# Kernel optimization log

Measured on AMD Instinct MI355X. Metric: run time of the kernel, lower is better.

Reference implementation:

```python
import jax, jax.numpy as jnp
import numpy as np

B, H, S, D = 4, 16, 2048, 64
DROPOUT_P = 0.5
INV_SCALE = np.sqrt(DROPOUT_P)  # module quirk: divides qk by sqrt(dropout_p)


def setup_inputs() -> dict:
    key = jax.random.key(0)
    kq, kk, kv, km = jax.random.split(key, 4)
    query = jax.random.normal(kq, (B, H, S, D), dtype=jnp.float32)
    key_t = jax.random.normal(kk, (B, H, S, D), dtype=jnp.float32)
    value = jax.random.normal(kv, (B, H, S, D), dtype=jnp.float32)
    # inverted dropout mask: keep with prob (1-p), scale kept entries by 1/(1-p)
    u = jax.random.uniform(km, (B, H, S, S), dtype=jnp.float32)
    dropout_mask = (u > DROPOUT_P).astype(jnp.float32) / (1.0 - DROPOUT_P)
    return {"query": query, "key_t": key_t, "value": value, "dropout_mask": dropout_mask}


def reference(query, key_t, value, dropout_mask):
    # qk = Q @ K^T, scaled by 1/inv_scale_factor  (inv_scale_factor = sqrt(0.5))
    qk = jnp.einsum("bhsd,bhtd->bhst", query, key_t) / INV_SCALE
    attn = jax.nn.softmax(qk, axis=-1)
    attn = attn * dropout_mask  # fused dropout (training mode, p=0.5)
    out = jnp.einsum("bhst,bhtd->bhsd", attn, value)
    return out
```

## Files before the change

### kernel.cpp

```cpp
#include <hip/hip_runtime.h>

#define Bn 4
#define Hn 16
#define Sn 2048
#define Dn 64
#define NT (Sn / 64)
#define BLOB 24576
#define WS_NEED ((size_t)Bn * Hn * NT * BLOB)

typedef __attribute__((ext_vector_type(8))) short bf16x8;
typedef __attribute__((ext_vector_type(4))) float f32x4;
typedef __attribute__((ext_vector_type(4))) float float4_t;

__device__ __forceinline__ short f2bf(float f) {
    union { float f; unsigned u; } v; v.f = f;
    unsigned r = v.u + 0x7fffu + ((v.u >> 16) & 1u);
    return (short)(r >> 16);
}
__device__ __forceinline__ float bf2f(short h) {
    union { unsigned u; float f; } v; v.u = ((unsigned)(unsigned short)h) << 16;
    return v.f;
}

__global__ __launch_bounds__(256) void prepass_kernel(
    const float* __restrict__ K, const float* __restrict__ V, char* __restrict__ ws)
{
    const int tid = threadIdx.x;
    const int kv0 = (blockIdx.x & (NT - 1)) * 64;
    char* blob = ws + (size_t)blockIdx.x * BLOB;
    const size_t kv_base = (size_t)(blockIdx.x >> 5) * Sn * Dn;

    {
        const int r  = tid >> 2;
        const int dc = (tid & 3) * 16;
        const float* krow = K + kv_base + (size_t)(kv0 + r) * Dn + dc;
        float4_t k0 = ((const float4_t*)krow)[0];
        float4_t k1 = ((const float4_t*)krow)[1];
        float4_t k2 = ((const float4_t*)krow)[2];
        float4_t k3 = ((const float4_t*)krow)[3];
        float fv[16] = {k0[0],k0[1],k0[2],k0[3], k1[0],k1[1],k1[2],k1[3],
                        k2[0],k2[1],k2[2],k2[3], k3[0],k3[1],k3[2],k3[3]};
        bf16x8 ha, hb, la, lb;
#pragma unroll
        for (int j = 0; j < 8; ++j) {
            short h = f2bf(fv[j]);
            ha[j] = h; la[j] = f2bf(fv[j] - bf2f(h));
            short h2 = f2bf(fv[j + 8]);
            hb[j] = h2; lb[j] = f2bf(fv[j + 8] - bf2f(h2));
        }
        const unsigned base = (unsigned)(r * 128 + dc * 2);
        const unsigned swz  = (unsigned)((r & 7) << 4);
        *(bf16x8*)(blob + ((base) ^ swz))             = ha;
        *(bf16x8*)(blob + ((base + 16) ^ swz))        = hb;
        *(bf16x8*)(blob + 8192 + ((base) ^ swz))      = la;
        *(bf16x8*)(blob + 8192 + ((base + 16) ^ swz)) = lb;
    }
    {
        const int r2 = (tid & 31) * 2;
        const int d0 = (tid >> 5) * 8;
        const float* v0 = V + kv_base + (size_t)(kv0 + r2) * Dn + d0;
        float4_t a0 = ((const float4_t*)v0)[0];
        float4_t a1 = ((const float4_t*)v0)[1];
        float4_t b0 = ((const float4_t*)(v0 + Dn))[0];
        float4_t b1 = ((const float4_t*)(v0 + Dn))[1];
        float av[8] = {a0[0],a0[1],a0[2],a0[3], a1[0],a1[1],a1[2],a1[3]};
        float bv[8] = {b0[0],b0[1],b0[2],b0[3], b1[0],b1[1],b1[2],b1[3]};
#pragma unroll
        for (int j = 0; j < 8; ++j) {
            const int d = d0 + j;
            unsigned wv = ((unsigned)(unsigned short)f2bf(av[j]))
                        | (((unsigned)(unsigned short)f2bf(bv[j])) << 16);
            unsigned off = ((unsigned)(d * 128 + r2 * 2)) ^ ((unsigned)((d & 7) << 4));
            *(unsigned*)(blob + 16384 + off) = wv;
        }
    }
}

__global__ __launch_bounds__(256) void attn_main_kernel(
    const float* __restrict__ Q, const float* __restrict__ Msk,
    const char* __restrict__ ws, float* __restrict__ Out)
{
    __shared__ char lds_kv[2][BLOB];
    __shared__ unsigned short lds_p[4][16 * 64];

    const int tid  = threadIdx.x;
    const int lane = tid & 63;
    const int w    = tid >> 6;
    const int lq   = lane & 15;
    const int lg   = lane >> 4;

    const int q0 = blockIdx.x * 64;
    const int bh = blockIdx.y;

    const float* qp = Q + (size_t)bh * Sn * Dn;
    const float* mbase = Msk + (size_t)bh * Sn * Sn + (size_t)(q0 + w * 16) * Sn;
    const char* ws_bh = ws + (size_t)bh * NT * BLOB;
    float* op = Out + (size_t)bh * Sn * Dn + (size_t)(q0 + w * 16) * Dn;

    const float QSCALE = 2.0402789f;

    bf16x8 qh[2], ql[2];
    {
        const float* qrow = qp + (size_t)(q0 + w * 16 + lq) * Dn + lg * 8;
#pragma unroll
        for (int c = 0; c < 2; ++c) {
            float4_t f0 = *(const float4_t*)(qrow + c * 32);
            float4_t f1 = *(const float4_t*)(qrow + c * 32 + 4);
            float fv[8] = {f0[0], f0[1], f0[2], f0[3], f1[0], f1[1], f1[2], f1[3]};
            bf16x8 th, tl;
#pragma unroll
            for (int j = 0; j < 8; ++j) {
                float x = fv[j] * QSCALE;
                short h = f2bf(x);
                th[j] = h;
                tl[j] = f2bf(x - bf2f(h));
            }
            qh[c] = th; ql[c] = tl;
        }
    }

    float l_st[4];
    f32x4 o_acc[4];
#pragma unroll
    for (int r = 0; r < 4; ++r) l_st[r] = 0.0f;
#pragma unroll
    for (int dt = 0; dt < 4; ++dt) o_acc[dt] = (f32x4){0.f, 0.f, 0.f, 0.f};

#define STAGE(TSRC, BUFIDX) do {                                                   \
        const char* _src = ws_bh + (size_t)(TSRC) * BLOB + w * 6144 + lane * 16;   \
        char* _dst = &lds_kv[BUFIDX][w * 6144];                                    \
        _Pragma("unroll")                                                          \
        for (int _i = 0; _i < 6; ++_i) {                                           \
            __builtin_amdgcn_global_load_lds(                                      \
                (const __attribute__((address_space(1))) void*)(_src + _i * 1024), \
                (__attribute__((address_space(3))) void*)(_dst + _i * 1024),       \
                16, 0, 0);                                                         \
        }                                                                          \
    } while (0)

#define LOADMASK(MREG, TSRC) do {                                                        \
        _Pragma("unroll")                                                                \
        for (int _r = 0; _r < 4; ++_r)                                                   \
        _Pragma("unroll")                                                                \
        for (int _kt = 0; _kt < 4; ++_kt)                                                \
            MREG[_r * 4 + _kt] =                                                         \
                mbase[(size_t)(lg * 4 + _r) * Sn + (TSRC) * 64 + _kt * 16 + lq];         \
    } while (0)

#define TILE_BARRIER() do {                                                        \
        asm volatile("s_waitcnt vmcnt(16)\n\ts_barrier" ::: "memory");             \
        __builtin_amdgcn_sched_barrier(0);                                         \
    } while (0)

#define ITER_BODY(T, BUF, MU, MP) do {                                                   \
        TILE_BARRIER();                 \
        if ((T) + 1 < NT) {                                                              \
            STAGE((T) + 1, (BUF) ^ 1);                                                   \
            __builtin_amdgcn_sched_barrier(0);       \
            LOADMASK(MP, (T) + 1);                                                       \
            __builtin_amdgcn_sched_barrier(0);          \
        }                                                                                \
        const char* kb = lds_kv[BUF];                                                    \
        f32x4 s[4];                                                                      \
        _Pragma("unroll")                                                                \
        for (int kt = 0; kt < 4; ++kt) {                                                 \
            f32x4 acc = (f32x4){0.f, 0.f, 0.f, 0.f};                                     \
            _Pragma("unroll")                                                            \
            for (int c = 0; c < 2; ++c) {                                                \
                const int krow = kt * 16 + lq;                                           \
                unsigned off = ((unsigned)(krow * 128 + (c * 32 + lg * 8) * 2))          \
                             ^ ((unsigned)((krow & 7) << 4));                            \
                bf16x8 khf = *(const bf16x8*)(kb + off);                                 \
                bf16x8 klf = *(const bf16x8*)(kb + 8192 + off);                          \
                acc = __builtin_amdgcn_mfma_f32_16x16x32_bf16(qh[c], khf, acc, 0, 0, 0); \
                acc = __builtin_amdgcn_mfma_f32_16x16x32_bf16(qh[c], klf, acc, 0, 0, 0); \
                acc = __builtin_amdgcn_mfma_f32_16x16x32_bf16(ql[c], khf, acc, 0, 0, 0); \
            }                                                                            \
            s[kt] = acc;                                                                 \
        }                                                                                \
                      \
        {                                                                                \
            unsigned short* pw = &lds_p[w][0];                                           \
            _Pragma("unroll")                                                            \
            for (int r = 0; r < 4; ++r) {                                                \
                const int row = lg * 4 + r;                                              \
                float psum = 0.f;                                                        \
                _Pragma("unroll")                                                        \
                for (int kt = 0; kt < 4; ++kt) {                                         \
                    float p = exp2f(s[kt][r]);                                           \
                    psum += p;                                                           \
                    float pm = p * MU[r * 4 + kt];                                       \
                    unsigned off = ((unsigned)(row * 128 + (kt * 16 + lq) * 2))          \
                                 ^ ((unsigned)((row & 7) << 4));                         \
                    *(unsigned short*)((char*)pw + off) = (unsigned short)f2bf(pm);      \
                }                                                                        \
                l_st[r] += psum;                                                         \
            }                                                                            \
        }                                                                                \
            \
        _Pragma("unroll")                                                                \
        for (int kc = 0; kc < 2; ++kc) {                                                 \
            unsigned poff = ((unsigned)(lq * 128 + (kc * 32 + lg * 8) * 2))              \
                          ^ ((unsigned)((lq & 7) << 4));                                 \
            bf16x8 pa = *(const bf16x8*)((const char*)&lds_p[w][0] + poff);              \
            _Pragma("unroll")                                                            \
            for (int dt = 0; dt < 4; ++dt) {                                             \
                const int drow = dt * 16 + lq;                                           \
                unsigned voff = ((unsigned)(drow * 128 + (kc * 32 + lg * 8) * 2))        \
                              ^ ((unsigned)((drow & 7) << 4));                           \
                bf16x8 vb = *(const bf16x8*)(kb + 16384 + voff);                         \
                o_acc[dt] = __builtin_amdgcn_mfma_f32_16x16x32_bf16(pa, vb, o_acc[dt],   \
                                                                    0, 0, 0);            \
            }                                                                            \
        }                                                                                \
    } while (0)

    float mA[16], mB[16];
    STAGE(0, 0);
    __builtin_amdgcn_sched_barrier(0);
    LOADMASK(mA, 0);
    __builtin_amdgcn_sched_barrier(0);

    for (int t = 0; t < NT; t += 2) {
        ITER_BODY(t, 0, mA, mB);
        ITER_BODY(t + 1, 1, mB, mA);
    }

#pragma unroll
    for (int r = 0; r < 4; ++r) {
        float ls = l_st[r];
        ls += __shfl_xor(ls, 1);
        ls += __shfl_xor(ls, 2);
        ls += __shfl_xor(ls, 4);
        ls += __shfl_xor(ls, 8);
        const float inv = 1.0f / ls;
#pragma unroll
        for (int dt = 0; dt < 4; ++dt) {
            op[(size_t)(lg * 4 + r) * Dn + dt * 16 + lq] = o_acc[dt][r] * inv;
        }
    }
#undef STAGE
#undef LOADMASK
#undef TILE_BARRIER
#undef ITER_BODY
}

__global__ __launch_bounds__(256) void attn_drop_fallback(
    const float* __restrict__ Q, const float* __restrict__ K,
    const float* __restrict__ V, const float* __restrict__ Msk,
    float* __restrict__ Out)
{
    __shared__ unsigned short lds_kh[64 * 64];
    __shared__ unsigned short lds_kl[64 * 64];
    __shared__ unsigned short lds_v[64 * 64];
    __shared__ unsigned short lds_p[4][16 * 64];

    const int tid  = threadIdx.x;
    const int lane = tid & 63;
    const int w    = tid >> 6;
    const int lq   = lane & 15;
    const int lg   = lane >> 4;
    const int q0 = blockIdx.x * 64;
    const int bh = blockIdx.y;
    const size_t qkv_base = (size_t)bh * Sn * Dn;
    const float* qp = Q + qkv_base;
    const float* kp = K + qkv_base;
    const float* vp = V + qkv_base;
    const float* mbase = Msk + (size_t)bh * Sn * Sn + (size_t)(q0 + w * 16) * Sn;
    float* op = Out + qkv_base + (size_t)(q0 + w * 16) * Dn;
    const float SQRT2 = 1.41421356237f;
    const float LOG2E = 1.44269504089f;

    bf16x8 qh[2], ql[2];
    {
        const float* qrow = qp + (size_t)(q0 + w * 16 + lq) * Dn + lg * 8;
#pragma unroll
        for (int c = 0; c < 2; ++c) {
            float4_t f0 = *(const float4_t*)(qrow + c * 32);
            float4_t f1 = *(const float4_t*)(qrow + c * 32 + 4);
            float fv[8] = {f0[0], f0[1], f0[2], f0[3], f1[0], f1[1], f1[2], f1[3]};
            bf16x8 th, tl;
#pragma unroll
            for (int j = 0; j < 8; ++j) {
                short h = f2bf(fv[j]);
                th[j] = h; tl[j] = f2bf(fv[j] - bf2f(h));
            }
            qh[c] = th; ql[c] = tl;
        }
    }
    float m_st[4], l_st[4];
    f32x4 o_acc[4];
#pragma unroll
    for (int r = 0; r < 4; ++r) { m_st[r] = -INFINITY; l_st[r] = 0.0f; }
#pragma unroll
    for (int dt = 0; dt < 4; ++dt) o_acc[dt] = (f32x4){0.f, 0.f, 0.f, 0.f};

    for (int t = 0; t < NT; ++t) {
        const int kv0 = t * 64;
        __syncthreads();
        {
            const int r  = tid >> 2;
            const int dc = (tid & 3) * 16;
            const float* krow = kp + (size_t)(kv0 + r) * Dn + dc;
            float4_t k0 = ((const float4_t*)krow)[0];
            float4_t k1 = ((const float4_t*)krow)[1];
            float4_t k2 = ((const float4_t*)krow)[2];
            float4_t k3 = ((const float4_t*)krow)[3];
            float fv[16] = {k0[0],k0[1],k0[2],k0[3], k1[0],k1[1],k1[2],k1[3],
                            k2[0],k2[1],k2[2],k2[3], k3[0],k3[1],k3[2],k3[3]};
            bf16x8 ha, hb, la, lb;
#pragma unroll
            for (int j = 0; j < 8; ++j) {
                short h = f2bf(fv[j]);
                ha[j] = h; la[j] = f2bf(fv[j] - bf2f(h));
                short h2 = f2bf(fv[j + 8]);
                hb[j] = h2; lb[j] = f2bf(fv[j + 8] - bf2f(h2));
            }
            const unsigned base = (unsigned)(r * 128 + dc * 2);
            const unsigned swz  = (unsigned)((r & 7) << 4);
            *(bf16x8*)((char*)lds_kh + ((base) ^ swz))      = ha;
            *(bf16x8*)((char*)lds_kh + ((base + 16) ^ swz)) = hb;
            *(bf16x8*)((char*)lds_kl + ((base) ^ swz))      = la;
            *(bf16x8*)((char*)lds_kl + ((base + 16) ^ swz)) = lb;
        }
        {
            const int r2 = (tid & 31) * 2;
            const int d0 = (tid >> 5) * 8;
            const float* v0 = vp + (size_t)(kv0 + r2) * Dn + d0;
            float4_t a0 = ((const float4_t*)v0)[0];
            float4_t a1 = ((const float4_t*)v0)[1];
            float4_t b0 = ((const float4_t*)(v0 + Dn))[0];
            float4_t b1 = ((const float4_t*)(v0 + Dn))[1];
            float av[8] = {a0[0],a0[1],a0[2],a0[3], a1[0],a1[1],a1[2],a1[3]};
            float bv[8] = {b0[0],b0[1],b0[2],b0[3], b1[0],b1[1],b1[2],b1[3]};
#pragma unroll
            for (int j = 0; j < 8; ++j) {
                const int d = d0 + j;
                unsigned wv = ((unsigned)(unsigned short)f2bf(av[j]))
                            | (((unsigned)(unsigned short)f2bf(bv[j])) << 16);
                unsigned off = ((unsigned)(d * 128 + r2 * 2)) ^ ((unsigned)((d & 7) << 4));
                *(unsigned*)((char*)lds_v + off) = wv;
            }
        }
        __syncthreads();
        f32x4 s[4];
#pragma unroll
        for (int kt = 0; kt < 4; ++kt) {
            f32x4 acc = (f32x4){0.f, 0.f, 0.f, 0.f};
#pragma unroll
            for (int c = 0; c < 2; ++c) {
                const int krow = kt * 16 + lq;
                unsigned off = ((unsigned)(krow * 128 + (c * 32 + lg * 8) * 2))
                             ^ ((unsigned)((krow & 7) << 4));
                bf16x8 khf = *(const bf16x8*)((const char*)lds_kh + off);
                bf16x8 klf = *(const bf16x8*)((const char*)lds_kl + off);
                acc = __builtin_amdgcn_mfma_f32_16x16x32_bf16(qh[c], khf, acc, 0, 0, 0);
                acc = __builtin_amdgcn_mfma_f32_16x16x32_bf16(qh[c], klf, acc, 0, 0, 0);
                acc = __builtin_amdgcn_mfma_f32_16x16x32_bf16(ql[c], khf, acc, 0, 0, 0);
            }
            s[kt] = acc * SQRT2;
        }
        float pbuf[4][4];
#pragma unroll
        for (int r = 0; r < 4; ++r) {
            float mx = fmaxf(fmaxf(s[0][r], s[1][r]), fmaxf(s[2][r], s[3][r]));
            mx = fmaxf(mx, __shfl_xor(mx, 1));
            mx = fmaxf(mx, __shfl_xor(mx, 2));
            mx = fmaxf(mx, __shfl_xor(mx, 4));
            mx = fmaxf(mx, __shfl_xor(mx, 8));
            const float mnew = fmaxf(m_st[r], mx);
            const float corr = exp2f((m_st[r] - mnew) * LOG2E);
            m_st[r] = mnew;
            float psum = 0.f;
#pragma unroll
            for (int kt = 0; kt < 4; ++kt) {
                float p = exp2f((s[kt][r] - mnew) * LOG2E);
                pbuf[kt][r] = p;
                psum += p;
            }
            l_st[r] = l_st[r] * corr + psum;
#pragma unroll
            for (int dt = 0; dt < 4; ++dt) o_acc[dt][r] *= corr;
        }
        {
            unsigned short* pw = &lds_p[w][0];
#pragma unroll
            for (int r = 0; r < 4; ++r) {
                const int row = lg * 4 + r;
                const float* mp = mbase + (size_t)row * Sn + kv0;
#pragma unroll
                for (int kt = 0; kt < 4; ++kt) {
                    float mv = mp[kt * 16 + lq];
                    float pm = pbuf[kt][r] * mv;
                    unsigned off = ((unsigned)(row * 128 + (kt * 16 + lq) * 2))
                                 ^ ((unsigned)((row & 7) << 4));
                    *(unsigned short*)((char*)pw + off) = (unsigned short)f2bf(pm);
                }
            }
        }
        __syncthreads();
#pragma unroll
        for (int kc = 0; kc < 2; ++kc) {
            unsigned poff = ((unsigned)(lq * 128 + (kc * 32 + lg * 8) * 2))
                          ^ ((unsigned)((lq & 7) << 4));
            bf16x8 pa = *(const bf16x8*)((const char*)&lds_p[w][0] + poff);
#pragma unroll
            for (int dt = 0; dt < 4; ++dt) {
                const int drow = dt * 16 + lq;
                unsigned voff = ((unsigned)(drow * 128 + (kc * 32 + lg * 8) * 2))
                              ^ ((unsigned)((drow & 7) << 4));
                bf16x8 vb = *(const bf16x8*)((const char*)lds_v + voff);
                o_acc[dt] = __builtin_amdgcn_mfma_f32_16x16x32_bf16(pa, vb, o_acc[dt], 0, 0, 0);
            }
        }
    }
#pragma unroll
    for (int r = 0; r < 4; ++r) {
        float ls = l_st[r];
        ls += __shfl_xor(ls, 1);
        ls += __shfl_xor(ls, 2);
        ls += __shfl_xor(ls, 4);
        ls += __shfl_xor(ls, 8);
        const float inv = 1.0f / ls;
#pragma unroll
        for (int dt = 0; dt < 4; ++dt) {
            op[(size_t)(lg * 4 + r) * Dn + dt * 16 + lq] = o_acc[dt][r] * inv;
        }
    }
}

extern "C" void kernel_launch(void* const* d_in, const int* in_sizes, int n_in,
                              void* d_out, int out_size, void* d_ws, size_t ws_size,
                              hipStream_t stream) {
    const float* q   = (const float*)d_in[0];
    const float* k   = (const float*)d_in[1];
    const float* v   = (const float*)d_in[2];
    const float* msk = (const float*)d_in[3];
    float* out = (float*)d_out;

    if (ws_size >= WS_NEED) {
        prepass_kernel<<<dim3(Bn * Hn * NT), dim3(256), 0, stream>>>(k, v, (char*)d_ws);
        attn_main_kernel<<<dim3(Sn / 64, Bn * Hn), dim3(256), 0, stream>>>(
            q, msk, (const char*)d_ws, out);
    } else {
        attn_drop_fallback<<<dim3(Sn / 64, Bn * Hn), dim3(256), 0, stream>>>(
            q, k, v, msk, out);
    }
}
```

Baseline: 338.7 us.

## Pre-swizzle K/V into MFMA fragment order and read directly from global

```diff
diff --git a/kernel.cpp b/kernel.cpp
--- a/kernel.cpp
+++ b/kernel.cpp
@@ -30,57 +30,46 @@
     char* blob = ws + (size_t)blockIdx.x * BLOB;
     const size_t kv_base = (size_t)(blockIdx.x >> 5) * Sn * Dn;
 
-    {
-        const int r  = tid >> 2;
-        const int dc = (tid & 3) * 16;
-        const float* krow = K + kv_base + (size_t)(kv0 + r) * Dn + dc;
-        float4_t k0 = ((const float4_t*)krow)[0];
-        float4_t k1 = ((const float4_t*)krow)[1];
-        float4_t k2 = ((const float4_t*)krow)[2];
-        float4_t k3 = ((const float4_t*)krow)[3];
-        float fv[16] = {k0[0],k0[1],k0[2],k0[3], k1[0],k1[1],k1[2],k1[3],
-                        k2[0],k2[1],k2[2],k2[3], k3[0],k3[1],k3[2],k3[3]};
-        bf16x8 ha, hb, la, lb;
+#pragma unroll
+    for (int i = 0; i < 2; ++i) {
+        const int s    = tid + 256 * i;
+        const int kt2c = s >> 6;
+        const int ln   = s & 63;
+        const int row  = (kt2c >> 1) * 16 + (ln & 15);
+        const int dc   = (kt2c & 1) * 32 + (ln >> 4) * 8;
+        const float* kr = K + kv_base + (size_t)(kv0 + row) * Dn + dc;
+        float4_t f0 = ((const float4_t*)kr)[0];
+        float4_t f1 = ((const float4_t*)kr)[1];
+        float fv[8] = {f0[0],f0[1],f0[2],f0[3], f1[0],f1[1],f1[2],f1[3]};
+        bf16x8 h8, l8;
 #pragma unroll
         for (int j = 0; j < 8; ++j) {
             short h = f2bf(fv[j]);
-            ha[j] = h; la[j] = f2bf(fv[j] - bf2f(h));
-            short h2 = f2bf(fv[j + 8]);
-            hb[j] = h2; lb[j] = f2bf(fv[j + 8] - bf2f(h2));
-        }
-        const unsigned base = (unsigned)(r * 128 + dc * 2);
-        const unsigned swz  = (unsigned)((r & 7) << 4);
-        *(bf16x8*)(blob + ((base) ^ swz))             = ha;
-        *(bf16x8*)(blob + ((base + 16) ^ swz))        = hb;
-        *(bf16x8*)(blob + 8192 + ((base) ^ swz))      = la;
-        *(bf16x8*)(blob + 8192 + ((base + 16) ^ swz)) = lb;
-    }
-    {
-        const int r2 = (tid & 31) * 2;
-        const int d0 = (tid >> 5) * 8;
-        const float* v0 = V + kv_base + (size_t)(kv0 + r2) * Dn + d0;
-        float4_t a0 = ((const float4_t*)v0)[0];
-        float4_t a1 = ((const float4_t*)v0)[1];
-        float4_t b0 = ((const float4_t*)(v0 + Dn))[0];
-        float4_t b1 = ((const float4_t*)(v0 + Dn))[1];
-        float av[8] = {a0[0],a0[1],a0[2],a0[3], a1[0],a1[1],a1[2],a1[3]};
-        float bv[8] = {b0[0],b0[1],b0[2],b0[3], b1[0],b1[1],b1[2],b1[3]};
-#pragma unroll
-        for (int j = 0; j < 8; ++j) {
-            const int d = d0 + j;
-            unsigned wv = ((unsigned)(unsigned short)f2bf(av[j]))
-                        | (((unsigned)(unsigned short)f2bf(bv[j])) << 16);
-            unsigned off = ((unsigned)(d * 128 + r2 * 2)) ^ ((unsigned)((d & 7) << 4));
-            *(unsigned*)(blob + 16384 + off) = wv;
-        }
-    }
-}
-
-__global__ __launch_bounds__(256) void attn_main_kernel(
+            h8[j] = h;
+            l8[j] = f2bf(fv[j] - bf2f(h));
+        }
+        *(bf16x8*)(blob + s * 16)        = h8;
+        *(bf16x8*)(blob + 8192 + s * 16) = l8;
+    }
+#pragma unroll
+    for (int i = 0; i < 2; ++i) {
+        const int s    = tid + 256 * i;
+        const int grp  = s >> 6;
+        const int ln   = s & 63;
+        const int kvb  = (grp >> 2) * 32 + (ln >> 4) * 8;
+        const int dcol = (grp & 3) * 16 + (ln & 15);
+        const float* vcol = V + kv_base + (size_t)(kv0 + kvb) * Dn + dcol;
+        bf16x8 v8;
+#pragma unroll
+        for (int j = 0; j < 8; ++j) v8[j] = f2bf(vcol[(size_t)j * Dn]);
+        *(bf16x8*)(blob + 16384 + s * 16) = v8;
+    }
+}
+
+__global__ __launch_bounds__(256) void attn_main_v4(
     const float* __restrict__ Q, const float* __restrict__ Msk,
     const char* __restrict__ ws, float* __restrict__ Out)
 {
-    __shared__ char lds_kv[2][BLOB];
     __shared__ unsigned short lds_p[4][16 * 64];
 
     const int tid  = threadIdx.x;
@@ -89,13 +78,13 @@
     const int lq   = lane & 15;
     const int lg   = lane >> 4;
 
-    const int q0 = blockIdx.x * 64;
-    const int bh = blockIdx.y;
-
-    const float* qp = Q + (size_t)bh * Sn * Dn;
+    const int bh = blockIdx.x;
+    const int q0 = blockIdx.y * 64;
+
+    const float* qp    = Q + (size_t)bh * Sn * Dn;
     const float* mbase = Msk + (size_t)bh * Sn * Sn + (size_t)(q0 + w * 16) * Sn;
-    const char* ws_bh = ws + (size_t)bh * NT * BLOB;
-    float* op = Out + (size_t)bh * Sn * Dn + (size_t)(q0 + w * 16) * Dn;
+    const char*  bbh   = ws + (size_t)bh * NT * BLOB;
+    float*       op    = Out + (size_t)bh * Sn * Dn + (size_t)(q0 + w * 16) * Dn;
 
     const float QSCALE = 2.0402789f;
 
@@ -125,18 +114,6 @@
     for (int r = 0; r < 4; ++r) l_st[r] = 0.0f;
 #pragma unroll
     for (int dt = 0; dt < 4; ++dt) o_acc[dt] = (f32x4){0.f, 0.f, 0.f, 0.f};
-
-#define STAGE(TSRC, BUFIDX) do {                                                   \
-        const char* _src = ws_bh + (size_t)(TSRC) * BLOB + w * 6144 + lane * 16;   \
-        char* _dst = &lds_kv[BUFIDX][w * 6144];                                    \
-        _Pragma("unroll")                                                          \
-        for (int _i = 0; _i < 6; ++_i) {                                           \
-            __builtin_amdgcn_global_load_lds(                                      \
-                (const __attribute__((address_space(1))) void*)(_src + _i * 1024), \
-                (__attribute__((address_space(3))) void*)(_dst + _i * 1024),       \
-                16, 0, 0);                                                         \
-        }                                                                          \
-    } while (0)
 
 #define LOADMASK(MREG, TSRC) do {                                                        \
         _Pragma("unroll")                                                                \
@@ -152,33 +129,29 @@
         __builtin_amdgcn_sched_barrier(0);                                         \
     } while (0)
 
-#define ITER_BODY(T, BUF, MU, MP) do {                                                   \
-        TILE_BARRIER();                 \
+#define ITER(T, MU, MP) do {                                                             \
+        TILE_BARRIER();                                                                  \
+        const char* bt = bbh + (size_t)(T) * BLOB;                                       \
         if ((T) + 1 < NT) {                                                              \
-            STAGE((T) + 1, (BUF) ^ 1);                                                   \
-            __builtin_amdgcn_sched_barrier(0);       \
-            LOADMASK(MP, (T) + 1);                                                       \
-            __builtin_amdgcn_sched_barrier(0);          \
+            LOADMASK(MP, (T) + 1);                       \
+            __builtin_amdgcn_sched_barrier(0);  \
         }                                                                                \
-        const char* kb = lds_kv[BUF];                                                    \
         f32x4 s[4];                                                                      \
         _Pragma("unroll")                                                                \
         for (int kt = 0; kt < 4; ++kt) {                                                 \
             f32x4 acc = (f32x4){0.f, 0.f, 0.f, 0.f};                                     \
             _Pragma("unroll")                                                            \
             for (int c = 0; c < 2; ++c) {                                                \
-                const int krow = kt * 16 + lq;                                           \
-                unsigned off = ((unsigned)(krow * 128 + (c * 32 + lg * 8) * 2))          \
-                             ^ ((unsigned)((krow & 7) << 4));                            \
-                bf16x8 khf = *(const bf16x8*)(kb + off);                                 \
-                bf16x8 klf = *(const bf16x8*)(kb + 8192 + off);                          \
+                const int fo = ((kt * 2 + c) * 64 + lane) * 16;                          \
+                bf16x8 khf = *(const bf16x8*)(bt + fo);                                  \
+                bf16x8 klf = *(const bf16x8*)(bt + 8192 + fo);                           \
                 acc = __builtin_amdgcn_mfma_f32_16x16x32_bf16(qh[c], khf, acc, 0, 0, 0); \
                 acc = __builtin_amdgcn_mfma_f32_16x16x32_bf16(qh[c], klf, acc, 0, 0, 0); \
                 acc = __builtin_amdgcn_mfma_f32_16x16x32_bf16(ql[c], khf, acc, 0, 0, 0); \
             }                                                                            \
             s[kt] = acc;                                                                 \
         }                                                                                \
-                      \
+                 \
         {                                                                                \
             unsigned short* pw = &lds_p[w][0];                                           \
             _Pragma("unroll")                                                            \
@@ -197,7 +170,7 @@
                 l_st[r] += psum;                                                         \
             }                                                                            \
         }                                                                                \
-            \
+           \
         _Pragma("unroll")                                                                \
         for (int kc = 0; kc < 2; ++kc) {                                                 \
             unsigned poff = ((unsigned)(lq * 128 + (kc * 32 + lg * 8) * 2))              \
@@ -205,10 +178,8 @@
             bf16x8 pa = *(const bf16x8*)((const char*)&lds_p[w][0] + poff);              \
             _Pragma("unroll")                                                            \
             for (int dt = 0; dt < 4; ++dt) {                                             \
-                const int drow = dt * 16 + lq;                                           \
-                unsigned voff = ((unsigned)(drow * 128 + (kc * 32 + lg * 8) * 2))        \
-                              ^ ((unsigned)((drow & 7) << 4));                           \
-                bf16x8 vb = *(const bf16x8*)(kb + 16384 + voff);                         \
+                bf16x8 vb = *(const bf16x8*)(bt + 16384 +                                \
+                                             (((kc * 4 + dt) * 64 + lane) * 16));        \
                 o_acc[dt] = __builtin_amdgcn_mfma_f32_16x16x32_bf16(pa, vb, o_acc[dt],   \
                                                                     0, 0, 0);            \
             }                                                                            \
@@ -216,14 +187,12 @@
     } while (0)
 
     float mA[16], mB[16];
-    STAGE(0, 0);
-    __builtin_amdgcn_sched_barrier(0);
     LOADMASK(mA, 0);
     __builtin_amdgcn_sched_barrier(0);
 
     for (int t = 0; t < NT; t += 2) {
-        ITER_BODY(t, 0, mA, mB);
-        ITER_BODY(t + 1, 1, mB, mA);
+        ITER(t, mA, mB);
+        ITER(t + 1, mB, mA);
     }
 
 #pragma unroll
@@ -239,10 +208,9 @@
             op[(size_t)(lg * 4 + r) * Dn + dt * 16 + lq] = o_acc[dt][r] * inv;
         }
     }
-#undef STAGE
 #undef LOADMASK
 #undef TILE_BARRIER
-#undef ITER_BODY
+#undef ITER
 }
 
 __global__ __launch_bounds__(256) void attn_drop_fallback(
@@ -440,7 +408,7 @@
 
     if (ws_size >= WS_NEED) {
         prepass_kernel<<<dim3(Bn * Hn * NT), dim3(256), 0, stream>>>(k, v, (char*)d_ws);
-        attn_main_kernel<<<dim3(Sn / 64, Bn * Hn), dim3(256), 0, stream>>>(
+        attn_main_v4<<<dim3(Bn * Hn, Sn / 64), dim3(256), 0, stream>>>(
             q, msk, (const char*)d_ws, out);
     } else {
         attn_drop_fallback<<<dim3(Sn / 64, Bn * Hn), dim3(256), 0, stream>>>(
```

Result: slower. 638.8 us (+88.6%).

## Transpose QK^T MFMA output to vectorize mask loads and P stores

Applied to the files above, without the earlier changes.

```diff
diff --git a/kernel.cpp b/kernel.cpp
--- a/kernel.cpp
+++ b/kernel.cpp
@@ -11,6 +11,7 @@
 typedef __attribute__((ext_vector_type(8))) short bf16x8;
 typedef __attribute__((ext_vector_type(4))) float f32x4;
 typedef __attribute__((ext_vector_type(4))) float float4_t;
+typedef __attribute__((ext_vector_type(2))) unsigned u32x2;
 
 __device__ __forceinline__ short f2bf(float f) {
     union { float f; unsigned u; } v; v.f = f;
@@ -20,6 +21,11 @@
 __device__ __forceinline__ float bf2f(short h) {
     union { unsigned u; float f; } v; v.u = ((unsigned)(unsigned short)h) << 16;
     return v.f;
+}
+__device__ __forceinline__ unsigned cvtpk_bf16(float a, float b) {
+    unsigned d;
+    asm("v_cvt_pk_bf16_f32 %0, %1, %2" : "=v"(d) : "v"(a), "v"(b));
+    return d;
 }
 
 __global__ __launch_bounds__(256) void prepass_kernel(
@@ -82,6 +88,7 @@
 {
     __shared__ char lds_kv[2][BLOB];
     __shared__ unsigned short lds_p[4][16 * 64];
+    __shared__ float lds_l[4][16];
 
     const int tid  = threadIdx.x;
     const int lane = tid & 63;
@@ -92,8 +99,8 @@
     const int q0 = blockIdx.x * 64;
     const int bh = blockIdx.y;
 
-    const float* qp = Q + (size_t)bh * Sn * Dn;
-    const float* mbase = Msk + (size_t)bh * Sn * Sn + (size_t)(q0 + w * 16) * Sn;
+    const float* qp   = Q + (size_t)bh * Sn * Dn;
+    const float* mrow = Msk + (size_t)bh * Sn * Sn + (size_t)(q0 + w * 16 + lq) * Sn;
     const char* ws_bh = ws + (size_t)bh * NT * BLOB;
     float* op = Out + (size_t)bh * Sn * Dn + (size_t)(q0 + w * 16) * Dn;
 
@@ -119,10 +126,8 @@
         }
     }
 
-    float l_st[4];
+    float l_acc = 0.0f;
     f32x4 o_acc[4];
-#pragma unroll
-    for (int r = 0; r < 4; ++r) l_st[r] = 0.0f;
 #pragma unroll
     for (int dt = 0; dt < 4; ++dt) o_acc[dt] = (f32x4){0.f, 0.f, 0.f, 0.f};
 
@@ -138,17 +143,14 @@
         }                                                                          \
     } while (0)
 
-#define LOADMASK(MREG, TSRC) do {                                                        \
-        _Pragma("unroll")                                                                \
-        for (int _r = 0; _r < 4; ++_r)                                                   \
-        _Pragma("unroll")                                                                \
-        for (int _kt = 0; _kt < 4; ++_kt)                                                \
-            MREG[_r * 4 + _kt] =                                                         \
-                mbase[(size_t)(lg * 4 + _r) * Sn + (TSRC) * 64 + _kt * 16 + lq];         \
+#define LOADMASK(MREG, TSRC) do {                                                  \
+        _Pragma("unroll")                                                          \
+        for (int _kt = 0; _kt < 4; ++_kt)                                          \
+            MREG[_kt] = *(const float4_t*)(mrow + (TSRC) * 64 + _kt * 16 + lg * 4);\
     } while (0)
 
 #define TILE_BARRIER() do {                                                        \
-        asm volatile("s_waitcnt vmcnt(16)\n\ts_barrier" ::: "memory");             \
+        asm volatile("s_waitcnt vmcnt(4)\n\ts_barrier" ::: "memory");              \
         __builtin_amdgcn_sched_barrier(0);                                         \
     } while (0)
 
@@ -172,32 +174,32 @@
                              ^ ((unsigned)((krow & 7) << 4));                            \
                 bf16x8 khf = *(const bf16x8*)(kb + off);                                 \
                 bf16x8 klf = *(const bf16x8*)(kb + 8192 + off);                          \
-                acc = __builtin_amdgcn_mfma_f32_16x16x32_bf16(qh[c], khf, acc, 0, 0, 0); \
-                acc = __builtin_amdgcn_mfma_f32_16x16x32_bf16(qh[c], klf, acc, 0, 0, 0); \
-                acc = __builtin_amdgcn_mfma_f32_16x16x32_bf16(ql[c], khf, acc, 0, 0, 0); \
+                                                    \
+                acc = __builtin_amdgcn_mfma_f32_16x16x32_bf16(khf, qh[c], acc, 0, 0, 0); \
+                acc = __builtin_amdgcn_mfma_f32_16x16x32_bf16(klf, qh[c], acc, 0, 0, 0); \
+                acc = __builtin_amdgcn_mfma_f32_16x16x32_bf16(khf, ql[c], acc, 0, 0, 0); \
             }                                                                            \
             s[kt] = acc;                                                                 \
         }                                                                                \
-                      \
+            \
         {                                                                                \
             unsigned short* pw = &lds_p[w][0];                                           \
+            const unsigned pswz = (unsigned)((lq & 7) << 4);                             \
             _Pragma("unroll")                                                            \
-            for (int r = 0; r < 4; ++r) {                                                \
-                const int row = lg * 4 + r;                                              \
-                float psum = 0.f;                                                        \
-                _Pragma("unroll")                                                        \
-                for (int kt = 0; kt < 4; ++kt) {                                         \
-                    float p = exp2f(s[kt][r]);                                           \
-                    psum += p;                                                           \
-                    float pm = p * MU[r * 4 + kt];                                       \
-                    unsigned off = ((unsigned)(row * 128 + (kt * 16 + lq) * 2))          \
-                                 ^ ((unsigned)((row & 7) << 4));                         \
-                    *(unsigned short*)((char*)pw + off) = (unsigned short)f2bf(pm);      \
-                }                                                                        \
-                l_st[r] += psum;                                                         \
+            for (int kt = 0; kt < 4; ++kt) {                                             \
+                float p0 = exp2f(s[kt][0]);                                              \
+                float p1 = exp2f(s[kt][1]);                                              \
+                float p2 = exp2f(s[kt][2]);                                              \
+                float p3 = exp2f(s[kt][3]);                                              \
+                l_acc += (p0 + p1) + (p2 + p3);                                          \
+                unsigned w0 = cvtpk_bf16(p0 * MU[kt][0], p1 * MU[kt][1]);                \
+                unsigned w1 = cvtpk_bf16(p2 * MU[kt][2], p3 * MU[kt][3]);                \
+                unsigned off = ((unsigned)(lq * 128 + kt * 32 + lg * 8)) ^ pswz;         \
+                u32x2 wv; wv[0] = w0; wv[1] = w1;                                        \
+                *(u32x2*)((char*)pw + off) = wv;                                         \
             }                                                                            \
         }                                                                                \
-            \
+                  \
         _Pragma("unroll")                                                                \
         for (int kc = 0; kc < 2; ++kc) {                                                 \
             unsigned poff = ((unsigned)(lq * 128 + (kc * 32 + lg * 8) * 2))              \
@@ -206,16 +208,17 @@
             _Pragma("unroll")                                                            \
             for (int dt = 0; dt < 4; ++dt) {                                             \
                 const int drow = dt * 16 + lq;                                           \
-                unsigned voff = ((unsigned)(drow * 128 + (kc * 32 + lg * 8) * 2))        \
-                              ^ ((unsigned)((drow & 7) << 4));                           \
-                bf16x8 vb = *(const bf16x8*)(kb + 16384 + voff);                         \
+                unsigned voff = 16384 +                                                  \
+                    (((unsigned)(drow * 128 + (kc * 32 + lg * 8) * 2))                   \
+                     ^ ((unsigned)((drow & 7) << 4)));                                   \
+                bf16x8 vb = *(const bf16x8*)(kb + voff);                                 \
                 o_acc[dt] = __builtin_amdgcn_mfma_f32_16x16x32_bf16(pa, vb, o_acc[dt],   \
                                                                     0, 0, 0);            \
             }                                                                            \
         }                                                                                \
     } while (0)
 
-    float mA[16], mB[16];
+    float4_t mA[4], mB[4];
     STAGE(0, 0);
     __builtin_amdgcn_sched_barrier(0);
     LOADMASK(mA, 0);
@@ -226,14 +229,13 @@
         ITER_BODY(t + 1, 1, mB, mA);
     }
 
+    l_acc += __shfl_xor(l_acc, 16);
+    l_acc += __shfl_xor(l_acc, 32);
+    if (lane < 16) lds_l[w][lane] = l_acc;
+    __builtin_amdgcn_sched_barrier(0);
 #pragma unroll
     for (int r = 0; r < 4; ++r) {
-        float ls = l_st[r];
-        ls += __shfl_xor(ls, 1);
-        ls += __shfl_xor(ls, 2);
-        ls += __shfl_xor(ls, 4);
-        ls += __shfl_xor(ls, 8);
-        const float inv = 1.0f / ls;
+        const float inv = 1.0f / lds_l[w][lg * 4 + r];
 #pragma unroll
         for (int dt = 0; dt < 4; ++dt) {
             op[(size_t)(lg * 4 + r) * Dn + dt * 16 + lq] = o_acc[dt][r] * inv;
```

Result: no change. 344.9 us (+1.8%).
